# Kernel optimization log

Hardware: AMD Instinct MI355X
Metric: run time of the kernel (lower is better)

Reference implementation:

```python
import jax, jax.numpy as jnp
import numpy as np

B, T, LD, HD, NH, NL = 8, 16, 256, 512, 8, 6
N = 65           # num_patches + 1 tokens per frame from encoder
AED = 64         # action_embed_dim
NDA = 11         # num_discrete_actions
MLP = 4 * HD


def _ln(x, g, b, eps=1e-5):
    m = jnp.mean(x, -1, keepdims=True)
    v = jnp.mean((x - m) ** 2, -1, keepdims=True)
    return (x - m) / jnp.sqrt(v + eps) * g + b


def setup_inputs() -> dict:
    key = jax.random.key(0)
    ks = iter(jax.random.split(key, 48))
    def nrm(shape):
        return jax.random.normal(next(ks), shape, jnp.float32) * 0.02
    inp = {
        'z_sequence': jax.random.normal(next(ks), (B, T, N, LD), jnp.float32),
        'continuous_actions': jax.random.normal(next(ks), (B, T, 2), jnp.float32),
        'discrete_actions': jax.random.randint(next(ks), (B, T), 0, NDA),
        'w_de': nrm((NDA, AED)),
        'w_cp': nrm((2, AED)), 'b_cp': jnp.zeros((AED,), jnp.float32),
        'w_ap': nrm((2 * AED, HD)), 'b_ap': jnp.zeros((HD,), jnp.float32),
        'w_tp': nrm((LD, HD)), 'b_tp': jnp.zeros((HD,), jnp.float32),
        'w_te': nrm((64, HD)),
        'ln1_g': jnp.ones((NL, HD), jnp.float32), 'ln1_b': jnp.zeros((NL, HD), jnp.float32),
        'wq': nrm((NL, HD, HD)), 'bq': jnp.zeros((NL, HD), jnp.float32),
        'wk': nrm((NL, HD, HD)), 'bk': jnp.zeros((NL, HD), jnp.float32),
        'wv': nrm((NL, HD, HD)), 'bv': jnp.zeros((NL, HD), jnp.float32),
        'wo': nrm((NL, HD, HD)), 'bo': jnp.zeros((NL, HD), jnp.float32),
        'ln2_g': jnp.ones((NL, HD), jnp.float32), 'ln2_b': jnp.zeros((NL, HD), jnp.float32),
        'w1': nrm((NL, HD, MLP)), 'b1': jnp.zeros((NL, MLP), jnp.float32),
        'w2': nrm((NL, MLP, HD)), 'b2': jnp.zeros((NL, HD), jnp.float32),
        'norm_g': jnp.ones((HD,), jnp.float32), 'norm_b': jnp.zeros((HD,), jnp.float32),
        'w_out': nrm((HD, LD)), 'b_out': jnp.zeros((LD,), jnp.float32),
        'residual_weight': jnp.float32(0.5),
    }
    return inp


def reference(z_sequence, continuous_actions, discrete_actions,
              w_de, w_cp, b_cp, w_ap, b_ap, w_tp, b_tp, w_te,
              ln1_g, ln1_b, wq, bq, wk, bk, wv, bv, wo, bo,
              ln2_g, ln2_b, w1, b1, w2, b2,
              norm_g, norm_b, w_out, b_out, residual_weight):
    Bq, Tq, Nq, Dq = z_sequence.shape
    hd = HD // NH
    scale = hd ** -0.5
    # --- per-timestep action + patch token embedding (vectorized over T) ---
    de = w_de[discrete_actions]                          # (B,T,AED)
    ce = continuous_actions @ w_cp + b_cp                # (B,T,AED)
    ac = jnp.concatenate([de, ce], -1)                   # (B,T,2*AED)
    at = (ac @ w_ap + b_ap)[:, :, None, :]               # (B,T,1,HD) action token
    pt = z_sequence @ w_tp + b_tp                        # (B,T,N,HD)
    te = w_te[:Tq][None, :, None, :]                     # (1,T,1,HD) time embedding
    x = jnp.concatenate([at + te, pt + te], axis=2)      # (B,T,1+N,HD) interleaved
    S = Tq * (Nq + 1)
    x = x.reshape(Bq, S, HD)
    # --- block-causal mask: True = cannot attend ---
    ts = jnp.repeat(jnp.arange(Tq), Nq + 1)
    mask = ts[None, :] > ts[:, None]                     # (S,S)

    def body(h, p):
        g1, be1, Wq, Bq_, Wk, Bk_, Wv, Bv_, Wo, Bo_, g2, be2, W1, B1, W2, B2 = p
        y = _ln(h, g1, be1)
        q = (y @ Wq + Bq_).reshape(Bq, S, NH, hd)
        k = (y @ Wk + Bk_).reshape(Bq, S, NH, hd)
        v = (y @ Wv + Bv_).reshape(Bq, S, NH, hd)
        sc = jnp.einsum('bqhd,bkhd->bhqk', q, k) * scale
        sc = jnp.where(mask[None, None], -jnp.inf, sc)
        a = jax.nn.softmax(sc, axis=-1)
        o = jnp.einsum('bhqk,bkhd->bqhd', a, v).reshape(Bq, S, HD)
        h = h + o @ Wo + Bo_
        y = _ln(h, g2, be2)
        h = h + jax.nn.gelu(y @ W1 + B1, approximate=False) @ W2 + B2
        return h, None

    x, _ = jax.lax.scan(body, x, (ln1_g, ln1_b, wq, bq, wk, bk, wv, bv, wo, bo,
                                  ln2_g, ln2_b, w1, b1, w2, b2))
    x = _ln(x, norm_g, norm_b)
    patch_out = x.reshape(Bq, Tq, Nq + 1, HD)[:, :, 1:, :] @ w_out + b_out
    alpha = jax.nn.sigmoid(residual_weight)
    return z_sequence + alpha * patch_out
```

## Files before the change

### kernel.cpp

```cpp
#include <hip/hip_runtime.h>
#include <hip/hip_bf16.h>
#include <cmath>

typedef __attribute__((ext_vector_type(8)))  __bf16 bf16x8;
typedef __attribute__((ext_vector_type(4)))  float  f32x4;
typedef __attribute__((ext_vector_type(16))) float  f32x16;
typedef const __attribute__((address_space(1))) void* as1cv;
typedef __attribute__((address_space(3))) void*       as3v;

static constexpr int BB = 8, TT = 16, NN = 65, LD = 256, HD = 512, NH = 8, NL = 6;
static constexpr int SS    = TT * (NN + 1);
static constexpr int ROWS  = BB * SS;
static constexpr int PROWS = BB * TT * NN;
static constexpr int MLPD  = 2048;

__global__ void transpose_cast(const float* __restrict__ in, __bf16* __restrict__ out,
                               int R, int C, size_t ibs, size_t obs)
{
  __shared__ float t[32][33];
  in  += ibs * blockIdx.z;
  out += obs * blockIdx.z;
  int bx = blockIdx.x * 32, by = blockIdx.y * 32;
  #pragma unroll
  for (int i = threadIdx.y; i < 32; i += 8)
    t[i][threadIdx.x] = in[(size_t)(by + i) * C + bx + threadIdx.x];
  __syncthreads();
  #pragma unroll
  for (int i = threadIdx.y; i < 32; i += 8)
    out[(size_t)(bx + i) * R + by + threadIdx.x] = (__bf16)t[threadIdx.x][i];
}

__global__ __launch_bounds__(256) void cast_bf16(const float* __restrict__ in,
                                                 __bf16* __restrict__ out)
{
  int i = (blockIdx.x * 256 + threadIdx.x) * 8;
  float4 a = *(const float4*)(in + i);
  float4 b = *(const float4*)(in + i + 4);
  bf16x8 o;
  o[0]=(__bf16)a.x; o[1]=(__bf16)a.y; o[2]=(__bf16)a.z; o[3]=(__bf16)a.w;
  o[4]=(__bf16)b.x; o[5]=(__bf16)b.y; o[6]=(__bf16)b.z; o[7]=(__bf16)b.w;
  *(bf16x8*)(out + i) = o;
}

__global__ void build_bqkv(const float* __restrict__ bq, const float* __restrict__ bk,
                           const float* __restrict__ bv, float* __restrict__ out)
{
  int i = blockIdx.x * 256 + threadIdx.x;
  int L = i / 1536, c = i % 1536;
  float v = (c < 512) ? bq[L*512 + c] : (c < 1024 ? bk[L*512 + c - 512] : bv[L*512 + c - 1024]);
  out[i] = v;
}

template<int FLAGS>
__global__ __launch_bounds__(256)
void gemm_bt(const __bf16* __restrict__ A, const __bf16* __restrict__ Bt,
             const float* __restrict__ bias, const float* __restrict__ resid,
             float* __restrict__ outF, __bf16* __restrict__ outB, __bf16* __restrict__ outB2,
             int M, int N, int K)
{
  __shared__ __bf16 As[64 * 64];
  __shared__ __bf16 Bs[128 * 64];
  const int tid = threadIdx.x;
  const int lane = tid & 63, w = tid >> 6;
  const int g = lane >> 4, cl = lane & 15;
  const int wr = w >> 1, wc = w & 1;
  const int gx = gridDim.x, nwg = gx * gridDim.y;
  const int orig = blockIdx.y * gx + blockIdx.x;
  const int q8 = nwg >> 3, r8 = nwg & 7;
  const int xcd = orig & 7, off = orig >> 3;
  const int tile = (xcd < r8 ? xcd * (q8 + 1) : r8 * (q8 + 1) + (xcd - r8) * q8) + off;
  const int tm = (tile / gx) * 64, tn = (tile % gx) * 128;

  f32x4 acc[2][4];
  const f32x4 zero4 = {0.f, 0.f, 0.f, 0.f};
  #pragma unroll
  for (int m = 0; m < 2; m++)
    #pragma unroll
    for (int n = 0; n < 4; n++) acc[m][n] = zero4;

  const int nk = K >> 6;
  for (int kt = 0; kt < nk; ++kt) {
    __syncthreads();
    const __bf16* Ag = A  + (size_t)tm * K + kt * 64;
    const __bf16* Bg = Bt + (size_t)tn * K + kt * 64;
    #pragma unroll
    for (int p = 0; p < 2; p++) {
      int c = p * 256 + tid;
      int row = c >> 3, j = c & 7;
      int jj = j ^ (row & 7);
      const __bf16* sa = Ag + (size_t)row * K + jj * 8;
      __builtin_amdgcn_global_load_lds((as1cv)sa, (as3v)&As[(p * 4 + w) * 512], 16, 0, 0);
    }
    #pragma unroll
    for (int p = 0; p < 4; p++) {
      int c = p * 256 + tid;
      int row = c >> 3, j = c & 7;
      int jj = j ^ (row & 7);
      const __bf16* sb = Bg + (size_t)row * K + jj * 8;
      __builtin_amdgcn_global_load_lds((as1cv)sb, (as3v)&Bs[(p * 4 + w) * 512], 16, 0, 0);
    }
    __syncthreads();
    #pragma unroll
    for (int kk = 0; kk < 2; kk++) {
      bf16x8 af[2], bfr[4];
      #pragma unroll
      for (int m = 0; m < 2; m++) {
        int row = wr * 32 + m * 16 + cl;
        af[m] = *(const bf16x8*)&As[row * 64 + ((kk * 4 + g) ^ (row & 7)) * 8];
      }
      #pragma unroll
      for (int n = 0; n < 4; n++) {
        int row = wc * 64 + n * 16 + cl;
        bfr[n] = *(const bf16x8*)&Bs[row * 64 + ((kk * 4 + g) ^ (row & 7)) * 8];
      }
      #pragma unroll
      for (int m = 0; m < 2; m++)
        #pragma unroll
        for (int n = 0; n < 4; n++)
          acc[m][n] = __builtin_amdgcn_mfma_f32_16x16x32_bf16(af[m], bfr[n], acc[m][n], 0, 0, 0);
    }
  }
  float bv[4];
  #pragma unroll
  for (int n = 0; n < 4; n++) bv[n] = bias[tn + wc * 64 + n * 16 + cl];
  #pragma unroll
  for (int m = 0; m < 2; m++) {
    int Rb = tm + wr * 32 + m * 16 + g * 4;
    #pragma unroll
    for (int i = 0; i < 4; i++) {
      int R = Rb + i;
      #pragma unroll
      for (int n = 0; n < 4; n++) {
        int C = tn + wc * 64 + n * 16 + cl;
        float v = acc[m][n][i] + bv[n];
        if (FLAGS & 1) v = 0.5f * v * (1.f + erff(v * 0.70710678118f));
        if (FLAGS & 2) v += resid[(size_t)R * N + C];
        if (FLAGS & 8) outF[(size_t)R * N + C] = v;
        if (FLAGS & 4) outB[(size_t)R * N + C] = (__bf16)v;
        if (FLAGS & 32) {
          if (C < 1024) {
            outB[(size_t)R * 1024 + C] = (__bf16)v;
          } else {
            int bb2 = R / SS, s2 = R % SS;
            int cc = C - 1024, hh = cc >> 6, dd = cc & 63;
            outB2[((size_t)((bb2 * NH + hh) * 64 + dd)) * SS + s2] = (__bf16)v;
          }
        }
      }
    }
  }
}

template<int FLAGS>
__global__ __launch_bounds__(256)
void gemm_n64(const __bf16* __restrict__ A, const __bf16* __restrict__ Bt,
              const float* __restrict__ bias, const float* __restrict__ resid,
              float* __restrict__ outF, __bf16* __restrict__ outB,
              int M, int N, int K)
{
  __shared__ __bf16 As[64 * 64];
  __shared__ __bf16 Bs[64 * 64];
  const int tid = threadIdx.x;
  const int lane = tid & 63, w = tid >> 6;
  const int g = lane >> 4, cl = lane & 15;
  const int wr = w >> 1, wc = w & 1;
  const int gx = gridDim.x, nwg = gx * gridDim.y;
  const int orig = blockIdx.y * gx + blockIdx.x;
  const int q8 = nwg >> 3, r8 = nwg & 7;
  const int xcd = orig & 7, off = orig >> 3;
  const int tile = (xcd < r8 ? xcd * (q8 + 1) : r8 * (q8 + 1) + (xcd - r8) * q8) + off;
  const int tm = (tile / gx) * 64, tn = (tile % gx) * 64;

  f32x4 acc[2][2];
  const f32x4 zero4 = {0.f, 0.f, 0.f, 0.f};
  #pragma unroll
  for (int m = 0; m < 2; m++)
    #pragma unroll
    for (int n = 0; n < 2; n++) acc[m][n] = zero4;

  const int nk = K >> 6;
  for (int kt = 0; kt < nk; ++kt) {
    __syncthreads();
    const __bf16* Ag = A  + (size_t)tm * K + kt * 64;
    const __bf16* Bg = Bt + (size_t)tn * K + kt * 64;
    #pragma unroll
    for (int p = 0; p < 2; p++) {
      int c = p * 256 + tid;
      int row = c >> 3, j = c & 7;
      int jj = j ^ (row & 7);
      const __bf16* sa = Ag + (size_t)row * K + jj * 8;
      const __bf16* sb = Bg + (size_t)row * K + jj * 8;
      __builtin_amdgcn_global_load_lds((as1cv)sa, (as3v)&As[(p * 4 + w) * 512], 16, 0, 0);
      __builtin_amdgcn_global_load_lds((as1cv)sb, (as3v)&Bs[(p * 4 + w) * 512], 16, 0, 0);
    }
    __syncthreads();
    #pragma unroll
    for (int kk = 0; kk < 2; kk++) {
      bf16x8 af[2], bfr[2];
      #pragma unroll
      for (int m = 0; m < 2; m++) {
        int row = wr * 32 + m * 16 + cl;
        af[m] = *(const bf16x8*)&As[row * 64 + ((kk * 4 + g) ^ (row & 7)) * 8];
      }
      #pragma unroll
      for (int n = 0; n < 2; n++) {
        int row = wc * 32 + n * 16 + cl;
        bfr[n] = *(const bf16x8*)&Bs[row * 64 + ((kk * 4 + g) ^ (row & 7)) * 8];
      }
      #pragma unroll
      for (int m = 0; m < 2; m++)
        #pragma unroll
        for (int n = 0; n < 2; n++)
          acc[m][n] = __builtin_amdgcn_mfma_f32_16x16x32_bf16(af[m], bfr[n], acc[m][n], 0, 0, 0);
    }
  }
  float bv[2];
  #pragma unroll
  for (int n = 0; n < 2; n++) bv[n] = bias[tn + wc * 32 + n * 16 + cl];
  #pragma unroll
  for (int m = 0; m < 2; m++) {
    int Rb = tm + wr * 32 + m * 16 + g * 4;
    #pragma unroll
    for (int i = 0; i < 4; i++) {
      int R = Rb + i;
      #pragma unroll
      for (int n = 0; n < 2; n++) {
        int C = tn + wc * 32 + n * 16 + cl;
        float v = acc[m][n][i] + bv[n];
        if (FLAGS & 1) v = 0.5f * v * (1.f + erff(v * 0.70710678118f));
        if (FLAGS & 2) v += resid[(size_t)R * N + C];
        if (FLAGS & 8) outF[(size_t)R * N + C] = v;
        if (FLAGS & 4) outB[(size_t)R * N + C] = (__bf16)v;
      }
    }
  }
}

__global__ __launch_bounds__(256) void ln_bf16(const float* __restrict__ in,
    const float* __restrict__ gam, const float* __restrict__ bet, __bf16* __restrict__ out)
{
  int w = threadIdx.x >> 6, l = threadIdx.x & 63;
  size_t row = (size_t)blockIdx.x * 4 + w;
  const float4* x4 = (const float4*)(in + row * HD);
  float4 v0 = x4[l], v1 = x4[l + 64];
  float s  = v0.x + v0.y + v0.z + v0.w + v1.x + v1.y + v1.z + v1.w;
  float q2 = v0.x*v0.x + v0.y*v0.y + v0.z*v0.z + v0.w*v0.w
           + v1.x*v1.x + v1.y*v1.y + v1.z*v1.z + v1.w*v1.w;
  #pragma unroll
  for (int m = 1; m < 64; m <<= 1) { s += __shfl_xor(s, m); q2 += __shfl_xor(q2, m); }
  float mean = s * (1.f / HD);
  float rstd = rsqrtf(q2 * (1.f / HD) - mean * mean + 1e-5f);
  int c0 = l * 4, c1 = 256 + l * 4;
  float4 g0 = *(const float4*)(gam + c0), g1 = *(const float4*)(gam + c1);
  float4 e0 = *(const float4*)(bet + c0), e1 = *(const float4*)(bet + c1);
  __bf16* o = out + row * HD;
  o[c0+0] = (__bf16)((v0.x-mean)*rstd*g0.x + e0.x);
  o[c0+1] = (__bf16)((v0.y-mean)*rstd*g0.y + e0.y);
  o[c0+2] = (__bf16)((v0.z-mean)*rstd*g0.z + e0.z);
  o[c0+3] = (__bf16)((v0.w-mean)*rstd*g0.w + e0.w);
  o[c1+0] = (__bf16)((v1.x-mean)*rstd*g1.x + e1.x);
  o[c1+1] = (__bf16)((v1.y-mean)*rstd*g1.y + e1.y);
  o[c1+2] = (__bf16)((v1.z-mean)*rstd*g1.z + e1.z);
  o[c1+3] = (__bf16)((v1.w-mean)*rstd*g1.w + e1.w);
}

__global__ __launch_bounds__(64) void act_embed(const float* __restrict__ cont,
    const int* __restrict__ disc, const float* __restrict__ w_de,
    const float* __restrict__ w_cp, const float* __restrict__ b_cp,
    const float* __restrict__ w_ap, const float* __restrict__ b_ap,
    const float* __restrict__ w_te, float* __restrict__ x)
{
  int t = blockIdx.x, b = blockIdx.y, l = threadIdx.x;
  int da = disc[b * TT + t];
  float c0 = cont[(b * TT + t) * 2], c1 = cont[(b * TT + t) * 2 + 1];
  int c = l * 8;
  float accv[8];
  #pragma unroll
  for (int j = 0; j < 8; j++) accv[j] = b_ap[c + j];
  for (int i = 0; i < 64; i++) {
    float ai = w_de[da * 64 + i];
    #pragma unroll
    for (int j = 0; j < 8; j++) accv[j] += ai * w_ap[i * HD + c + j];
  }
  for (int i = 0; i < 64; i++) {
    float ce = c0 * w_cp[i] + c1 * w_cp[64 + i] + b_cp[i];
    #pragma unroll
    for (int j = 0; j < 8; j++) accv[j] += ce * w_ap[(64 + i) * HD + c + j];
  }
  #pragma unroll
  for (int j = 0; j < 8; j++)
    x[((size_t)(b * SS) + t * 66) * HD + c + j] = accv[j] + w_te[t * HD + c + j];
}

__global__ __launch_bounds__(256) void assemble_patch(const float* __restrict__ pt,
    const float* __restrict__ te, float* __restrict__ x)
{
  int idx = (blockIdx.x * 256 + threadIdx.x) * 4;
  int c = idx & (HD - 1);
  int r = idx >> 9;
  int n = r % NN; int bt = r / NN; int t = bt & (TT - 1); int bb = bt >> 4;
  float4 v  = *(const float4*)(pt + idx);
  float4 tv = *(const float4*)(te + t * HD + c);
  v.x += tv.x; v.y += tv.y; v.z += tv.z; v.w += tv.w;
  *(float4*)(x + ((size_t)(bb * SS + t * 66 + 1 + n)) * HD + c) = v;
}

__device__ inline unsigned pkbf(float lo, float hi2) {
  unsigned short a = __builtin_bit_cast(unsigned short, (__bf16)lo);
  unsigned short b = __builtin_bit_cast(unsigned short, (__bf16)hi2);
  return (unsigned)a | ((unsigned)b << 16);
}

__global__ __launch_bounds__(256) void attn_fwd(const __bf16* __restrict__ qk,
    const __bf16* __restrict__ vT, __bf16* __restrict__ o)
{
  const int w = threadIdx.x >> 6, lane = threadIdx.x & 63;
  const int lin = (blockIdx.x & 7) * 264 + (blockIdx.x >> 3);
  const int b   = lin / 264;
  const int rem = lin % 264;
  const int h = rem / 33, qt = rem % 33;
  const int l31 = lane & 31, hi = lane >> 5;
  const int q = qt * 32 + l31;
  const int kend = (q / 66 + 1) * 66;
  const int nkv = (((qt * 32 + 31) / 66 + 1) * 66 + 31) >> 5;

  __shared__ float red[4][32];
  __shared__ float lmS[4][32], llS[4][32];
  __shared__ float laS[3][64][32];
  __shared__ float red2[32][8];

  bf16x8 qf[4];
  const __bf16* qbase = qk + (size_t)(b * SS + q) * 1024 + h * 64 + hi * 8;
  #pragma unroll
  for (int s = 0; s < 4; s++) qf[s] = *(const bf16x8*)(qbase + s * 16);

  const f32x16 z16 = {0,0,0,0,0,0,0,0,0,0,0,0,0,0,0,0};
  f32x16 accA = z16, accB = z16;
  float m = -1e30f, lsum = 0.f;

  for (int kb = w; kb < nkv; kb += 4) {
    const int K0 = kb * 32;
    const __bf16* kbase = qk + (size_t)(b * SS + K0 + l31) * 1024 + 512 + h * 64 + hi * 8;
    bf16x8 kf0 = *(const bf16x8*)(kbase);
    bf16x8 kf1 = *(const bf16x8*)(kbase + 16);
    bf16x8 kf2 = *(const bf16x8*)(kbase + 32);
    bf16x8 kf3 = *(const bf16x8*)(kbase + 48);
    const __bf16* vbase = vT + (size_t)((b * NH + h) * 64 + l31) * SS + K0 + hi * 8;
    bf16x8 vf00 = *(const bf16x8*)(vbase);
    bf16x8 vf10 = *(const bf16x8*)(vbase + 16);
    bf16x8 vf01 = *(const bf16x8*)(vbase + (size_t)32 * SS);
    bf16x8 vf11 = *(const bf16x8*)(vbase + (size_t)32 * SS + 16);

    f32x16 st = z16;
    st = __builtin_amdgcn_mfma_f32_32x32x16_bf16(kf0, qf[0], st, 0, 0, 0);
    st = __builtin_amdgcn_mfma_f32_32x32x16_bf16(kf1, qf[1], st, 0, 0, 0);
    st = __builtin_amdgcn_mfma_f32_32x32x16_bf16(kf2, qf[2], st, 0, 0, 0);
    st = __builtin_amdgcn_mfma_f32_32x32x16_bf16(kf3, qf[3], st, 0, 0, 0);

    float p[16];
    #pragma unroll
    for (int r = 0; r < 16; r++) {
      int kg = K0 + (r & 3) + 8 * (r >> 2) + 4 * hi;
      p[r] = (kg < kend) ? st[r] * 0.125f : -1e30f;
    }
    float mx = fmaxf(fmaxf(fmaxf(p[0],p[1]),fmaxf(p[2],p[3])),
                     fmaxf(fmaxf(p[4],p[5]),fmaxf(p[6],p[7])));
    mx = fmaxf(mx, fmaxf(fmaxf(fmaxf(p[8],p[9]),fmaxf(p[10],p[11])),
                         fmaxf(fmaxf(p[12],p[13]),fmaxf(p[14],p[15]))));
    mx = fmaxf(mx, __shfl_xor(mx, 32));
    if (__any(mx > m + 8.f)) {
      float nm = fmaxf(m, mx);
      float alp = __expf(m - nm);
      m = nm; lsum *= alp;
      if (lane < 32) red[w][lane] = alp;
      asm volatile("s_waitcnt lgkmcnt(0)" ::: "memory");
      float4 a0 = *(const float4*)&red[w][hi * 4];
      float4 a1 = *(const float4*)&red[w][hi * 4 + 8];
      float4 a2 = *(const float4*)&red[w][hi * 4 + 16];
      float4 a3 = *(const float4*)&red[w][hi * 4 + 24];
      float afv[16] = {a0.x,a0.y,a0.z,a0.w, a1.x,a1.y,a1.z,a1.w,
                       a2.x,a2.y,a2.z,a2.w, a3.x,a3.y,a3.z,a3.w};
      #pragma unroll
      for (int r = 0; r < 16; r++) { accA[r] *= afv[r]; accB[r] *= afv[r]; }
    }
    float rs;
    #pragma unroll
    for (int r = 0; r < 16; r++) p[r] = __expf(p[r] - m);
    rs = ((p[0]+p[1])+(p[2]+p[3])) + ((p[4]+p[5])+(p[6]+p[7]))
       + ((p[8]+p[9])+(p[10]+p[11])) + ((p[12]+p[13])+(p[14]+p[15]));
    rs += __shfl_xor(rs, 32);
    lsum += rs;
    unsigned a0p = pkbf(p[0], p[1]),  a1p = pkbf(p[2], p[3]);
    unsigned a2p = pkbf(p[4], p[5]),  a3p = pkbf(p[6], p[7]);
    unsigned b0p = pkbf(p[8], p[9]),  b1p = pkbf(p[10], p[11]);
    unsigned b2p = pkbf(p[12], p[13]), b3p = pkbf(p[14], p[15]);
    unsigned s0 = __shfl_xor(a0p, 32), s1 = __shfl_xor(a1p, 32);
    unsigned s2 = __shfl_xor(a2p, 32), s3 = __shfl_xor(a3p, 32);
    unsigned t0 = __shfl_xor(b0p, 32), t1 = __shfl_xor(b1p, 32);
    unsigned t2 = __shfl_xor(b2p, 32), t3 = __shfl_xor(b3p, 32);
    union { unsigned u[4]; bf16x8 v; } af0, af1;
    af0.u[0] = hi ? s2 : a0p;  af0.u[1] = hi ? s3 : a1p;
    af0.u[2] = hi ? a2p : s0;  af0.u[3] = hi ? a3p : s1;
    af1.u[0] = hi ? t2 : b0p;  af1.u[1] = hi ? t3 : b1p;
    af1.u[2] = hi ? b2p : t0;  af1.u[3] = hi ? b3p : t1;
    accA = __builtin_amdgcn_mfma_f32_32x32x16_bf16(af0.v, vf00, accA, 0, 0, 0);
    accA = __builtin_amdgcn_mfma_f32_32x32x16_bf16(af1.v, vf10, accA, 0, 0, 0);
    accB = __builtin_amdgcn_mfma_f32_32x32x16_bf16(af0.v, vf01, accB, 0, 0, 0);
    accB = __builtin_amdgcn_mfma_f32_32x32x16_bf16(af1.v, vf11, accB, 0, 0, 0);
  }

  if (lane < 32) { lmS[w][lane] = m; llS[w][lane] = lsum; }
  if (w > 0) {
    #pragma unroll
    for (int r = 0; r < 16; r++) {
      laS[w - 1][lane][r]      = accA[r];
      laS[w - 1][lane][16 + r] = accB[r];
    }
  }
  __syncthreads();
  if (w != 0) return;
  float m0 = lmS[0][l31], m1 = lmS[1][l31], m2 = lmS[2][l31], m3 = lmS[3][l31];
  float M = fmaxf(fmaxf(m0, m1), fmaxf(m2, m3));
  float f0 = __expf(m0 - M), f1 = __expf(m1 - M);
  float f2 = __expf(m2 - M), f3 = __expf(m3 - M);
  float L = llS[0][l31] * f0 + llS[1][l31] * f1 + llS[2][l31] * f2 + llS[3][l31] * f3;
  if (lane < 32) {
    red2[lane][0] = f0; red2[lane][1] = f1;
    red2[lane][2] = f2; red2[lane][3] = f3;
    red2[lane][4] = 1.f / L;
  }
  asm volatile("s_waitcnt lgkmcnt(0)" ::: "memory");
  __bf16* obase = o + (size_t)(b * SS + qt * 32) * HD + h * 64 + l31;
  #pragma unroll
  for (int r = 0; r < 16; r++) {
    int qr = (r & 3) + 8 * (r >> 2) + 4 * hi;
    float4 fv = *(const float4*)&red2[qr][0];
    float il = red2[qr][4];
    float oa = (accA[r] * fv.x + laS[0][lane][r] * fv.y
              + laS[1][lane][r] * fv.z + laS[2][lane][r] * fv.w) * il;
    float ob = (accB[r] * fv.x + laS[0][lane][16 + r] * fv.y
              + laS[1][lane][16 + r] * fv.z + laS[2][lane][16 + r] * fv.w) * il;
    obase[(size_t)qr * HD]      = (__bf16)oa;
    obase[(size_t)qr * HD + 32] = (__bf16)ob;
  }
}

__global__ __launch_bounds__(256) void final_add(const float* __restrict__ z,
    const float* __restrict__ po, const float* __restrict__ rw, float* __restrict__ out)
{
  int idx = (blockIdx.x * 256 + threadIdx.x) * 4;
  int ld = idx & (LD - 1);
  int r = idx >> 8;
  int n = r % NN; int bt = r / NN; int t = bt & (TT - 1); int bb = bt >> 4;
  float alpha = 1.f / (1.f + __expf(-rw[0]));
  float4 zv = *(const float4*)(z + idx);
  float4 pv = *(const float4*)(po + ((size_t)(bb * SS + t * 66 + 1 + n)) * LD + ld);
  float4 ov;
  ov.x = zv.x + alpha * pv.x; ov.y = zv.y + alpha * pv.y;
  ov.z = zv.z + alpha * pv.z; ov.w = zv.w + alpha * pv.w;
  *(float4*)(out + idx) = ov;
}

extern "C" void kernel_launch(void* const* d_in, const int* in_sizes, int n_in,
                              void* d_out, int out_size, void* d_ws, size_t ws_size,
                              hipStream_t stream)
{
  const float* z    = (const float*)d_in[0];
  const float* cont = (const float*)d_in[1];
  const int*   disc = (const int*)d_in[2];
  const float* w_de = (const float*)d_in[3];
  const float* w_cp = (const float*)d_in[4];
  const float* b_cp = (const float*)d_in[5];
  const float* w_ap = (const float*)d_in[6];
  const float* b_ap = (const float*)d_in[7];
  const float* w_tp = (const float*)d_in[8];
  const float* b_tp = (const float*)d_in[9];
  const float* w_te = (const float*)d_in[10];
  const float* ln1g = (const float*)d_in[11];
  const float* ln1b = (const float*)d_in[12];
  const float* wq   = (const float*)d_in[13];
  const float* bq   = (const float*)d_in[14];
  const float* wk   = (const float*)d_in[15];
  const float* bk   = (const float*)d_in[16];
  const float* wv   = (const float*)d_in[17];
  const float* bv   = (const float*)d_in[18];
  const float* wo   = (const float*)d_in[19];
  const float* bo   = (const float*)d_in[20];
  const float* ln2g = (const float*)d_in[21];
  const float* ln2b = (const float*)d_in[22];
  const float* w1   = (const float*)d_in[23];
  const float* b1   = (const float*)d_in[24];
  const float* w2   = (const float*)d_in[25];
  const float* b2   = (const float*)d_in[26];
  const float* nog  = (const float*)d_in[27];
  const float* nob  = (const float*)d_in[28];
  const float* wout = (const float*)d_in[29];
  const float* bout = (const float*)d_in[30];
  const float* rw   = (const float*)d_in[31];
  float* out = (float*)d_out;

  char* p = (char*)d_ws;
  auto alloc = [&](size_t bytes) -> char* {
    char* r = p; p += (bytes + 255) & ~(size_t)255; return r;
  };
  __bf16* wqkvt = (__bf16*)alloc((size_t)NL * 1536 * 512 * 2);
  __bf16* wot_  = (__bf16*)alloc((size_t)NL * 512 * 512 * 2);
  __bf16* w1t   = (__bf16*)alloc((size_t)NL * 512 * 2048 * 2);
  __bf16* w2t   = (__bf16*)alloc((size_t)NL * 512 * 2048 * 2);
  __bf16* wtpt  = (__bf16*)alloc((size_t)512 * 256 * 2);
  __bf16* woutt = (__bf16*)alloc((size_t)256 * 512 * 2);
  float*  bqkv  = (float*)alloc((size_t)NL * 1536 * 4);
  __bf16* zbf   = (__bf16*)alloc((size_t)PROWS * LD * 2);
  float*  x     = (float*)alloc((size_t)ROWS * HD * 4);
  __bf16* y     = (__bf16*)alloc((size_t)ROWS * HD * 2);
  __bf16* qkb   = (__bf16*)alloc((size_t)ROWS * 1024 * 2);
  __bf16* vtb   = (__bf16*)alloc((size_t)ROWS * HD * 2);
  __bf16* ob    = (__bf16*)alloc((size_t)ROWS * HD * 2);
  __bf16* mid   = (__bf16*)alloc((size_t)ROWS * MLPD * 2);
  float*  ptb   = (float*)alloc((size_t)PROWS * HD * 4);
  (void)in_sizes; (void)n_in; (void)out_size; (void)ws_size;

  dim3 tb(32, 8);
  transpose_cast<<<dim3(16, 16, 6), tb, 0, stream>>>(wq, wqkvt,          512,  512,  262144, 786432);
  transpose_cast<<<dim3(16, 16, 6), tb, 0, stream>>>(wk, wqkvt + 262144, 512,  512,  262144, 786432);
  transpose_cast<<<dim3(16, 16, 6), tb, 0, stream>>>(wv, wqkvt + 524288, 512,  512,  262144, 786432);
  transpose_cast<<<dim3(16, 16, 6), tb, 0, stream>>>(wo, wot_,           512,  512,  262144, 262144);
  transpose_cast<<<dim3(64, 16, 6), tb, 0, stream>>>(w1, w1t,            512,  2048, 1048576, 1048576);
  transpose_cast<<<dim3(16, 64, 6), tb, 0, stream>>>(w2, w2t,            2048, 512,  1048576, 1048576);
  transpose_cast<<<dim3(16, 8, 1),  tb, 0, stream>>>(w_tp, wtpt,         256,  512,  0, 0);
  transpose_cast<<<dim3(8, 16, 1),  tb, 0, stream>>>(wout, woutt,        512,  256,  0, 0);
  build_bqkv<<<36, 256, 0, stream>>>(bq, bk, bv, bqkv);
  cast_bf16<<<(PROWS * LD) / 2048, 256, 0, stream>>>(z, zbf);

  gemm_n64<8><<<dim3(8, PROWS / 64), 256, 0, stream>>>(zbf, wtpt, b_tp, nullptr, ptb, nullptr,
                                                       PROWS, 512, 256);
  act_embed<<<dim3(16, 8), 64, 0, stream>>>(cont, disc, w_de, w_cp, b_cp, w_ap, b_ap, w_te, x);
  assemble_patch<<<(PROWS * HD) / 1024, 256, 0, stream>>>(ptb, w_te, x);

  for (int L = 0; L < NL; ++L) {
    ln_bf16<<<ROWS / 4, 256, 0, stream>>>(x, ln1g + L*HD, ln1b + L*HD, y);
    gemm_bt<32><<<dim3(12, ROWS / 64), 256, 0, stream>>>(y, wqkvt + (size_t)L*786432,
                                                         bqkv + L*1536, nullptr, nullptr,
                                                         qkb, vtb, ROWS, 1536, 512);
    attn_fwd<<<2112, 256, 0, stream>>>(qkb, vtb, ob);
    gemm_n64<10><<<dim3(8, ROWS / 64), 256, 0, stream>>>(ob, wot_ + (size_t)L*262144, bo + L*HD,
                                                         x, x, nullptr, ROWS, 512, 512);
    ln_bf16<<<ROWS / 4, 256, 0, stream>>>(x, ln2g + L*HD, ln2b + L*HD, y);
    gemm_bt<5><<<dim3(16, ROWS / 64), 256, 0, stream>>>(y, w1t + (size_t)L*1048576, b1 + L*MLPD,
                                                        nullptr, nullptr, mid, nullptr,
                                                        ROWS, 2048, 512);
    gemm_n64<10><<<dim3(8, ROWS / 64), 256, 0, stream>>>(mid, w2t + (size_t)L*1048576, b2 + L*HD,
                                                         x, x, nullptr, ROWS, 512, 2048);
  }
  ln_bf16<<<ROWS / 4, 256, 0, stream>>>(x, nog, nob, y);
  gemm_n64<8><<<dim3(4, ROWS / 64), 256, 0, stream>>>(y, woutt, bout, nullptr, ptb, nullptr,
                                                      ROWS, 256, 512);
  final_add<<<(PROWS * LD) / 1024, 256, 0, stream>>>(z, ptb, rw, out);
}
```

Measured before the change: 1.045 ms.

## Fuse final residual add into output GEMM, use exp2 softmax, pad attention LDS

The final projection GEMM now writes z + sigmoid(rw)*proj directly to the output, dropping the separate final_add kernel and its intermediate buffer round trip. In attention, the scale is pre-multiplied by log2(e) so exp2f replaces __expf, with the rescale threshold adjusted to match. The laS and red2 shared arrays are padded to reduce bank conflicts. The fused epilogue does a scattered, less-coalesced read of z and write of out per element.

```diff
diff --git a/kernel.cpp b/kernel.cpp
--- a/kernel.cpp
+++ b/kernel.cpp
@@ -156,7 +156,8 @@
 void gemm_n64(const __bf16* __restrict__ A, const __bf16* __restrict__ Bt,
               const float* __restrict__ bias, const float* __restrict__ resid,
               float* __restrict__ outF, __bf16* __restrict__ outB,
-              int M, int N, int K)
+              int M, int N, int K,
+              const float* __restrict__ zf, const float* __restrict__ rwp)
 {
   __shared__ __bf16 As[64 * 64];
   __shared__ __bf16 Bs[64 * 64];
@@ -214,6 +215,7 @@
           acc[m][n] = __builtin_amdgcn_mfma_f32_16x16x32_bf16(af[m], bfr[n], acc[m][n], 0, 0, 0);
     }
   }
+  const float alphaF = (FLAGS & 64) ? 1.f / (1.f + __expf(-rwp[0])) : 0.f;
   float bv[2];
   #pragma unroll
   for (int n = 0; n < 2; n++) bv[n] = bias[tn + wc * 32 + n * 16 + cl];
@@ -231,6 +233,14 @@
         if (FLAGS & 2) v += resid[(size_t)R * N + C];
         if (FLAGS & 8) outF[(size_t)R * N + C] = v;
         if (FLAGS & 4) outB[(size_t)R * N + C] = (__bf16)v;
+        if (FLAGS & 64) {
+          int bb2 = R / SS, s2 = R % SS;
+          int t = s2 / 66, k = s2 % 66;
+          if (k > 0) {
+            size_t oi = ((size_t)((bb2 * TT + t) * NN + (k - 1))) * LD + C;
+            outF[oi] = zf[oi] + alphaF * v;
+          }
+        }
       }
     }
   }
@@ -323,11 +333,12 @@
   const int q = qt * 32 + l31;
   const int kend = (q / 66 + 1) * 66;
   const int nkv = (((qt * 32 + 31) / 66 + 1) * 66 + 31) >> 5;
+  const float SCL = 0.125f * 1.44269504f;
 
   __shared__ float red[4][32];
   __shared__ float lmS[4][32], llS[4][32];
-  __shared__ float laS[3][64][32];
-  __shared__ float red2[32][8];
+  __shared__ float laS[3][64][33];
+  __shared__ float red2[32][9];
 
   bf16x8 qf[4];
   const __bf16* qbase = qk + (size_t)(b * SS + q) * 1024 + h * 64 + hi * 8;
@@ -361,16 +372,16 @@
     #pragma unroll
     for (int r = 0; r < 16; r++) {
       int kg = K0 + (r & 3) + 8 * (r >> 2) + 4 * hi;
-      p[r] = (kg < kend) ? st[r] * 0.125f : -1e30f;
+      p[r] = (kg < kend) ? st[r] * SCL : -1e30f;
     }
     float mx = fmaxf(fmaxf(fmaxf(p[0],p[1]),fmaxf(p[2],p[3])),
                      fmaxf(fmaxf(p[4],p[5]),fmaxf(p[6],p[7])));
     mx = fmaxf(mx, fmaxf(fmaxf(fmaxf(p[8],p[9]),fmaxf(p[10],p[11])),
                          fmaxf(fmaxf(p[12],p[13]),fmaxf(p[14],p[15]))));
     mx = fmaxf(mx, __shfl_xor(mx, 32));
-    if (__any(mx > m + 8.f)) {
+    if (__any(mx > m + 11.5416f)) {
       float nm = fmaxf(m, mx);
-      float alp = __expf(m - nm);
+      float alp = exp2f(m - nm);
       m = nm; lsum *= alp;
       if (lane < 32) red[w][lane] = alp;
       asm volatile("s_waitcnt lgkmcnt(0)" ::: "memory");
@@ -385,7 +396,7 @@
     }
     float rs;
     #pragma unroll
-    for (int r = 0; r < 16; r++) p[r] = __expf(p[r] - m);
+    for (int r = 0; r < 16; r++) p[r] = exp2f(p[r] - m);
     rs = ((p[0]+p[1])+(p[2]+p[3])) + ((p[4]+p[5])+(p[6]+p[7]))
        + ((p[8]+p[9])+(p[10]+p[11])) + ((p[12]+p[13])+(p[14]+p[15]));
     rs += __shfl_xor(rs, 32);
@@ -421,8 +432,8 @@
   if (w != 0) return;
   float m0 = lmS[0][l31], m1 = lmS[1][l31], m2 = lmS[2][l31], m3 = lmS[3][l31];
   float M = fmaxf(fmaxf(m0, m1), fmaxf(m2, m3));
-  float f0 = __expf(m0 - M), f1 = __expf(m1 - M);
-  float f2 = __expf(m2 - M), f3 = __expf(m3 - M);
+  float f0 = exp2f(m0 - M), f1 = exp2f(m1 - M);
+  float f2 = exp2f(m2 - M), f3 = exp2f(m3 - M);
   float L = llS[0][l31] * f0 + llS[1][l31] * f1 + llS[2][l31] * f2 + llS[3][l31] * f3;
   if (lane < 32) {
     red2[lane][0] = f0; red2[lane][1] = f1;
@@ -443,22 +454,6 @@
     obase[(size_t)qr * HD]      = (__bf16)oa;
     obase[(size_t)qr * HD + 32] = (__bf16)ob;
   }
-}
-
-__global__ __launch_bounds__(256) void final_add(const float* __restrict__ z,
-    const float* __restrict__ po, const float* __restrict__ rw, float* __restrict__ out)
-{
-  int idx = (blockIdx.x * 256 + threadIdx.x) * 4;
-  int ld = idx & (LD - 1);
-  int r = idx >> 8;
-  int n = r % NN; int bt = r / NN; int t = bt & (TT - 1); int bb = bt >> 4;
-  float alpha = 1.f / (1.f + __expf(-rw[0]));
-  float4 zv = *(const float4*)(z + idx);
-  float4 pv = *(const float4*)(po + ((size_t)(bb * SS + t * 66 + 1 + n)) * LD + ld);
-  float4 ov;
-  ov.x = zv.x + alpha * pv.x; ov.y = zv.y + alpha * pv.y;
-  ov.z = zv.z + alpha * pv.z; ov.w = zv.w + alpha * pv.w;
-  *(float4*)(out + idx) = ov;
 }
 
 extern "C" void kernel_launch(void* const* d_in, const int* in_sizes, int n_in,
@@ -533,7 +528,7 @@
   cast_bf16<<<(PROWS * LD) / 2048, 256, 0, stream>>>(z, zbf);
 
   gemm_n64<8><<<dim3(8, PROWS / 64), 256, 0, stream>>>(zbf, wtpt, b_tp, nullptr, ptb, nullptr,
-                                                       PROWS, 512, 256);
+                                                       PROWS, 512, 256, nullptr, nullptr);
   act_embed<<<dim3(16, 8), 64, 0, stream>>>(cont, disc, w_de, w_cp, b_cp, w_ap, b_ap, w_te, x);
   assemble_patch<<<(PROWS * HD) / 1024, 256, 0, stream>>>(ptb, w_te, x);
 
@@ -544,16 +539,17 @@
                                                          qkb, vtb, ROWS, 1536, 512);
     attn_fwd<<<2112, 256, 0, stream>>>(qkb, vtb, ob);
     gemm_n64<10><<<dim3(8, ROWS / 64), 256, 0, stream>>>(ob, wot_ + (size_t)L*262144, bo + L*HD,
-                                                         x, x, nullptr, ROWS, 512, 512);
+                                                         x, x, nullptr, ROWS, 512, 512,
+                                                         nullptr, nullptr);
     ln_bf16<<<ROWS / 4, 256, 0, stream>>>(x, ln2g + L*HD, ln2b + L*HD, y);
     gemm_bt<5><<<dim3(16, ROWS / 64), 256, 0, stream>>>(y, w1t + (size_t)L*1048576, b1 + L*MLPD,
                                                         nullptr, nullptr, mid, nullptr,
                                                         ROWS, 2048, 512);
     gemm_n64<10><<<dim3(8, ROWS / 64), 256, 0, stream>>>(mid, w2t + (size_t)L*1048576, b2 + L*HD,
-                                                         x, x, nullptr, ROWS, 512, 2048);
+                                                         x, x, nullptr, ROWS, 512, 2048,
+                                                         nullptr, nullptr);
   }
   ln_bf16<<<ROWS / 4, 256, 0, stream>>>(x, nog, nob, y);
-  gemm_n64<8><<<dim3(4, ROWS / 64), 256, 0, stream>>>(y, woutt, bout, nullptr, ptb, nullptr,
-                                                      ROWS, 256, 512);
-  final_add<<<(PROWS * LD) / 1024, 256, 0, stream>>>(z, ptb, rw, out);
-}
+  gemm_n64<64><<<dim3(4, ROWS / 64), 256, 0, stream>>>(y, woutt, bout, nullptr, out, nullptr,
+                                                       ROWS, 256, 512, z, rw);
+}
```

Result: no change. 1.040 ms, median of 2 (-0.4%).
